# Optimization experiments

Measured on AMD Instinct MI355X. Metric: run time of the kernel, lower is better.

Reference implementation:

```python
import jax, jax.numpy as jnp
import numpy as np

EMBED_DIM = 128
NUM_HEADS = 16
D_K = EMBED_DIM // NUM_HEADS  # n_wires per head = 8
DEPTH = 1
DIM = 2 ** D_K  # 256 state amplitudes


def _cnot_chain_inverse_perm(d, depth):
    """Inverse permutation of basis states under `depth` rounds of the CNOT ladder
    CNOT(0,1),...,CNOT(d-2,d-1),CNOT(d-1,0). Wire 0 = most significant bit."""
    idx = np.arange(2 ** d)
    shifts = d - 1 - np.arange(d)
    bits = (idx[:, None] >> shifts) & 1  # (2^d, d)
    for _ in range(depth):
        for w in range(d - 1):
            bits[:, w + 1] ^= bits[:, w]
        bits[:, 0] ^= bits[:, d - 1]
    fwd = (bits << shifts).sum(axis=1)  # psi'[fwd[b]] = psi[b]
    inv = np.empty_like(fwd)
    inv[fwd] = idx  # psi'[j] = psi[inv[j]]
    return inv


def _pauliz_signs(d):
    idx = np.arange(2 ** d)
    shifts = d - 1 - np.arange(d)
    bits = (idx[:, None] >> shifts) & 1
    return (1.0 - 2.0 * bits).astype(np.float32)  # (2^d, d)


_INV_PERM = jnp.asarray(_cnot_chain_inverse_perm(D_K, DEPTH))
_SIGNS = jnp.asarray(_pauliz_signs(D_K))


def quantum_head(angles):
    """angles: (..., d) RX rotation angles. Returns PauliZ expectations (..., d).

    Product state amplitudes after per-wire RX from |0..0>: probabilities are
    products of cos^2/sin^2; CNOT ladder is a basis permutation; <Z_w> is a
    signed sum of probabilities."""
    half = angles * 0.5
    c2 = jnp.cos(half) ** 2
    s2 = jnp.sin(half) ** 2
    lead = angles.shape[:-1]
    p = jnp.ones(lead + (1,), angles.dtype)
    for w in range(D_K):  # builds (..., 2^d) probability vector
        pair = jnp.stack([c2[..., w], s2[..., w]], axis=-1)
        p = (p[..., :, None] * pair[..., None, :]).reshape(lead + (-1,))
    p = p[..., _INV_PERM]  # apply CNOT ladder permutation
    return p @ _SIGNS  # (..., d) PauliZ expectations


def setup_inputs() -> dict:
    key = jax.random.key(0)
    ks = jax.random.split(key, 10)
    B, S, E = 8, 512, EMBED_DIM
    sc = 1.0 / np.sqrt(E)
    return {
        "x": jax.random.normal(ks[0], (B, S, E), jnp.float32),
        "Wq": jax.random.normal(ks[1], (E, E), jnp.float32) * sc,
        "bq": jnp.zeros((E,), jnp.float32),
        "Wk": jax.random.normal(ks[2], (E, E), jnp.float32) * sc,
        "bk": jnp.zeros((E,), jnp.float32),
        "Wv": jax.random.normal(ks[3], (E, E), jnp.float32) * sc,
        "bv": jnp.zeros((E,), jnp.float32),
        "Wo": jax.random.normal(ks[4], (E, E), jnp.float32) * sc,
        "bo": jnp.zeros((E,), jnp.float32),
        "theta": jax.random.normal(ks[5], (NUM_HEADS, D_K), jnp.float32),
    }


def reference(x, Wq, bq, Wk, bk, Wv, bv, Wo, bo, theta):
    B, S, E = x.shape
    H, dk = NUM_HEADS, D_K

    def split_heads(y):  # (B,S,E) -> (B,H,S,dk)
        return y.reshape(B, S, H, dk).transpose(0, 2, 1, 3)

    q = split_heads(x @ Wq + bq)
    k = split_heads(x @ Wk + bk)
    v = split_heads(x @ Wv + bv)

    th = theta[None, :, None, :]  # broadcast per-head trainable RX angles
    qh = quantum_head(q + th)
    kh = quantum_head(k + th)
    vh = quantum_head(v + th)

    scores = jnp.einsum("bhsd,bhtd->bhst", qh, kh) / jnp.sqrt(jnp.asarray(dk, x.dtype))
    attn = jax.nn.softmax(scores, axis=-1)
    out = jnp.einsum("bhst,bhtd->bhsd", attn, vh)
    out = out.transpose(0, 2, 1, 3).reshape(B, S, E)
    return out @ Wo + bo
```

## Files before the change

### kernel.cpp

```cpp
#include <hip/hip_runtime.h>
#include <hip/hip_bf16.h>
#include <math.h>

#define BB 8
#define SS 512
#define EE 128
#define HH 16
#define DKK 8

#define FMA4(ACC, S, W) do { (ACC).x += (S)*(W).x; (ACC).y += (S)*(W).y; \
                             (ACC).z += (S)*(W).z; (ACC).w += (S)*(W).w; } while(0)

__global__ __launch_bounds__(256) void k_qkvq(
    const float* __restrict__ x,
    const float* __restrict__ Wq, const float* __restrict__ bq,
    const float* __restrict__ Wk, const float* __restrict__ bk,
    const float* __restrict__ Wv, const float* __restrict__ bv,
    const float* __restrict__ theta,
    float* __restrict__ qh, float* __restrict__ kh, float* __restrict__ vh)
{
    __shared__ float xs[16][128];
    const int t = threadIdx.x;
    const int m = blockIdx.y;
    const int row0 = blockIdx.x * 16;

    {
        const float4* xv = (const float4*)(x + (size_t)row0 * 128);
        float4* xsv = (float4*)&xs[0][0];
        xsv[t]       = xv[t];
        xsv[t + 256] = xv[t + 256];
    }
    __syncthreads();

    const int cg   = t & 31;
    const int col0 = cg * 4;
    const int rg   = t >> 5;
    const int r0   = rg * 2;

    const float* __restrict__ W  = (m == 0) ? Wq : (m == 1) ? Wk : Wv;
    const float* __restrict__ bb = (m == 0) ? bq : (m == 1) ? bk : bv;
    float* __restrict__ outp     = (m == 0) ? qh : (m == 1) ? kh : vh;

    float4 acc0 = *(const float4*)&bb[col0];
    float4 acc1 = acc0;

    #pragma unroll 4
    for (int k4 = 0; k4 < 32; ++k4) {
        const float4 xa = ((const float4*)xs[r0 + 0])[k4];
        const float4 xb = ((const float4*)xs[r0 + 1])[k4];
        const float4 w0 = *(const float4*)&W[(k4 * 4 + 0) * 128 + col0];
        const float4 w1 = *(const float4*)&W[(k4 * 4 + 1) * 128 + col0];
        const float4 w2 = *(const float4*)&W[(k4 * 4 + 2) * 128 + col0];
        const float4 w3 = *(const float4*)&W[(k4 * 4 + 3) * 128 + col0];
        FMA4(acc0, xa.x, w0); FMA4(acc0, xa.y, w1);
        FMA4(acc0, xa.z, w2); FMA4(acc0, xa.w, w3);
        FMA4(acc1, xb.x, w0); FMA4(acc1, xb.y, w1);
        FMA4(acc1, xb.z, w2); FMA4(acc1, xb.w, w3);
    }

    const float4 th = *(const float4*)&theta[col0];
    const int h    = cg >> 1;
    const int half = cg & 1;

    float4 accs[2] = {acc0, acc1};
    #pragma unroll
    for (int r = 0; r < 2; ++r) {
        float4 c;
        c.x = __cosf(accs[r].x + th.x);
        c.y = __cosf(accs[r].y + th.y);
        c.z = __cosf(accs[r].z + th.z);
        c.w = __cosf(accs[r].w + th.w);
        const float p0 = c.x;
        const float p1 = p0 * c.y;
        const float p2 = p1 * c.z;
        const float p3 = p2 * c.w;
        const float recv = __shfl_xor(p3, 1);
        float4 o;
        if (half == 0) {
            const float s123 = c.y * c.z * c.w;
            o.x = s123 * recv;
            o.y = p1;
            o.z = p2;
            o.w = p3;
        } else {
            o.x = recv * p0;
            o.y = recv * p1;
            o.z = recv * p2;
            o.w = recv * p3;
        }
        const int g  = row0 + r0 + r;
        const int b_ = g >> 9;
        const int s  = g & 511;
        *(float4*)&outp[(((size_t)b_ * HH + h) * SS + s) * DKK + half * 4] = o;
    }
}

__global__ __launch_bounds__(256) void k_attn(
    const float* __restrict__ qh, const float* __restrict__ kh,
    const float* __restrict__ vh, float* __restrict__ hid)
{
    __shared__ float smem[12288];
    float4* kk = (float4*)smem;
    float4* vv = (float4*)smem + 1024;
    float (*part)[256][12] = (float (*)[256][12])smem;

    const int t  = threadIdx.x;
    const int L  = t & 63;
    const int wv = __builtin_amdgcn_readfirstlane(t >> 6);
    const int bh = blockIdx.x >> 1;
    const int q0 = (blockIdx.x & 1) * 256;
    const int h  = bh & 15;
    const int b_ = bh >> 4;

    {
        const float4* kg = (const float4*)kh + (size_t)bh * 1024;
        const float4* vg = (const float4*)vh + (size_t)bh * 1024;
        #pragma unroll
        for (int i = 0; i < 4; ++i) {
            kk[t + 256 * i] = kg[t + 256 * i];
            vv[t + 256 * i] = vg[t + 256 * i];
        }
    }

    float4 qa[4], qb[4];
    {
        const float4* qg = (const float4*)qh + ((size_t)bh * 512 + q0) * 2;
        #pragma unroll
        for (int rr = 0; rr < 4; ++rr) {
            qa[rr] = qg[(rr * 64 + L) * 2];
            qb[rr] = qg[(rr * 64 + L) * 2 + 1];
        }
    }
    __syncthreads();

    float4 accA[4], accB[4];
    float  den[4];
    #pragma unroll
    for (int rr = 0; rr < 4; ++rr) {
        accA[rr] = make_float4(0.f, 0.f, 0.f, 0.f);
        accB[rr] = make_float4(0.f, 0.f, 0.f, 0.f);
        den[rr]  = 0.f;
    }
    const float scale = 0.35355339059327373f;
    const float4* kbase = kk + wv * 256;
    const float4* vbase = vv + wv * 256;

    #pragma unroll 2
    for (int j = 0; j < 128; ++j) {
        const float4 k0 = kbase[2 * j];
        const float4 k1 = kbase[2 * j + 1];
        const float4 v0 = vbase[2 * j];
        const float4 v1 = vbase[2 * j + 1];
        #pragma unroll
        for (int rr = 0; rr < 4; ++rr) {
            const float s = qa[rr].x*k0.x + qa[rr].y*k0.y + qa[rr].z*k0.z + qa[rr].w*k0.w
                          + qb[rr].x*k1.x + qb[rr].y*k1.y + qb[rr].z*k1.z + qb[rr].w*k1.w;
            const float e = __expf(s * scale);
            den[rr] += e;
            FMA4(accA[rr], e, v0);
            FMA4(accB[rr], e, v1);
        }
    }
    __syncthreads();

    #pragma unroll
    for (int rr = 0; rr < 4; ++rr) {
        float* p = &part[wv][rr * 64 + L][0];
        ((float4*)p)[0] = accA[rr];
        ((float4*)p)[1] = accB[rr];
        p[8] = den[rr];
    }
    __syncthreads();

    {
        float4 rA = make_float4(0.f, 0.f, 0.f, 0.f);
        float4 rB = make_float4(0.f, 0.f, 0.f, 0.f);
        float  rd = 0.f;
        #pragma unroll
        for (int wq = 0; wq < 4; ++wq) {
            const float* p = &part[wq][t][0];
            const float4 a = ((const float4*)p)[0];
            const float4 b = ((const float4*)p)[1];
            rA.x += a.x; rA.y += a.y; rA.z += a.z; rA.w += a.w;
            rB.x += b.x; rB.y += b.y; rB.z += b.z; rB.w += b.w;
            rd   += p[8];
        }
        const float inv = 1.0f / rd;
        rA.x *= inv; rA.y *= inv; rA.z *= inv; rA.w *= inv;
        rB.x *= inv; rB.y *= inv; rB.z *= inv; rB.w *= inv;
        float* o = hid + ((size_t)(b_ * 512 + q0 + t)) * 128 + h * 8;
        ((float4*)o)[0] = rA;
        ((float4*)o)[1] = rB;
    }
}

__global__ __launch_bounds__(256) void k_out(
    const float* __restrict__ hid, const float* __restrict__ Wo,
    const float* __restrict__ bo, float* __restrict__ out)
{
    __shared__ float hs[16][128];
    const int t = threadIdx.x;
    const int row0 = blockIdx.x * 16;

    {
        const float4* hv = (const float4*)(hid + (size_t)row0 * 128);
        float4* hsv = (float4*)&hs[0][0];
        hsv[t]       = hv[t];
        hsv[t + 256] = hv[t + 256];
    }
    __syncthreads();

    const int cg   = t & 31;
    const int col0 = cg * 4;
    const int rg   = t >> 5;
    const int r0   = rg * 2;

    float4 acc0 = *(const float4*)&bo[col0];
    float4 acc1 = acc0;

    #pragma unroll 4
    for (int k4 = 0; k4 < 32; ++k4) {
        const float4 xa = ((const float4*)hs[r0 + 0])[k4];
        const float4 xb = ((const float4*)hs[r0 + 1])[k4];
        const float4 w0 = *(const float4*)&Wo[(k4 * 4 + 0) * 128 + col0];
        const float4 w1 = *(const float4*)&Wo[(k4 * 4 + 1) * 128 + col0];
        const float4 w2 = *(const float4*)&Wo[(k4 * 4 + 2) * 128 + col0];
        const float4 w3 = *(const float4*)&Wo[(k4 * 4 + 3) * 128 + col0];
        FMA4(acc0, xa.x, w0); FMA4(acc0, xa.y, w1);
        FMA4(acc0, xa.z, w2); FMA4(acc0, xa.w, w3);
        FMA4(acc1, xb.x, w0); FMA4(acc1, xb.y, w1);
        FMA4(acc1, xb.z, w2); FMA4(acc1, xb.w, w3);
    }

    *(float4*)&out[(size_t)(row0 + r0 + 0) * 128 + col0] = acc0;
    *(float4*)&out[(size_t)(row0 + r0 + 1) * 128 + col0] = acc1;
}

extern "C" void kernel_launch(void* const* d_in, const int* in_sizes, int n_in,
                              void* d_out, int out_size, void* d_ws, size_t ws_size,
                              hipStream_t stream)
{
    const float* x     = (const float*)d_in[0];
    const float* Wq    = (const float*)d_in[1];
    const float* bq    = (const float*)d_in[2];
    const float* Wk    = (const float*)d_in[3];
    const float* bk    = (const float*)d_in[4];
    const float* Wv    = (const float*)d_in[5];
    const float* bv    = (const float*)d_in[6];
    const float* Wo    = (const float*)d_in[7];
    const float* bo    = (const float*)d_in[8];
    const float* theta = (const float*)d_in[9];
    float* out = (float*)d_out;

    float* ws  = (float*)d_ws;
    float* qh  = ws;
    float* kh  = ws + 524288;
    float* vh  = ws + 1048576;
    float* hid = ws + 1572864;

    k_qkvq<<<dim3(256, 3), 256, 0, stream>>>(x, Wq, bq, Wk, bk, Wv, bv,
                                             theta, qh, kh, vh);
    k_attn<<<256, 256, 0, stream>>>(qh, kh, vh, hid);
    k_out <<<256, 256, 0, stream>>>(hid, Wo, bo, out);
}
```

Baseline: 52.34 us.

## Split attention keys across blocks and merge partial sums in output projection

Attention now launches 512 blocks, each handling a quarter of the keys for all 512 queries of one batch-head. Each wave writes unnormalized partial numerators and denominators to global memory, and the output-projection kernel sums the 16 partials per row before the matmul. The QKV kernel drops its shared-memory staging of x and reads rows directly from global memory, and launch-bounds hints are added. This buys more parallelism for the attention stage, but adds a large partial-sum buffer (about 50 MB written and read back) and raises register pressure from 8 query rows per thread.

```diff
diff --git a/kernel.cpp b/kernel.cpp
--- a/kernel.cpp
+++ b/kernel.cpp
@@ -11,7 +11,7 @@
 #define FMA4(ACC, S, W) do { (ACC).x += (S)*(W).x; (ACC).y += (S)*(W).y; \
                              (ACC).z += (S)*(W).z; (ACC).w += (S)*(W).w; } while(0)
 
-__global__ __launch_bounds__(256) void k_qkvq(
+__global__ __launch_bounds__(256, 3) void k_qkvq(
     const float* __restrict__ x,
     const float* __restrict__ Wq, const float* __restrict__ bq,
     const float* __restrict__ Wk, const float* __restrict__ bk,
@@ -19,18 +19,9 @@
     const float* __restrict__ theta,
     float* __restrict__ qh, float* __restrict__ kh, float* __restrict__ vh)
 {
-    __shared__ float xs[16][128];
     const int t = threadIdx.x;
     const int m = blockIdx.y;
     const int row0 = blockIdx.x * 16;
-
-    {
-        const float4* xv = (const float4*)(x + (size_t)row0 * 128);
-        float4* xsv = (float4*)&xs[0][0];
-        xsv[t]       = xv[t];
-        xsv[t + 256] = xv[t + 256];
-    }
-    __syncthreads();
 
     const int cg   = t & 31;
     const int col0 = cg * 4;
@@ -41,13 +32,15 @@
     const float* __restrict__ bb = (m == 0) ? bq : (m == 1) ? bk : bv;
     float* __restrict__ outp     = (m == 0) ? qh : (m == 1) ? kh : vh;
 
+    const float4* xr = (const float4*)(x + (size_t)(row0 + r0) * 128);
+
     float4 acc0 = *(const float4*)&bb[col0];
     float4 acc1 = acc0;
 
     #pragma unroll 4
     for (int k4 = 0; k4 < 32; ++k4) {
-        const float4 xa = ((const float4*)xs[r0 + 0])[k4];
-        const float4 xb = ((const float4*)xs[r0 + 1])[k4];
+        const float4 xa = xr[k4];
+        const float4 xb = xr[32 + k4];
         const float4 w0 = *(const float4*)&W[(k4 * 4 + 0) * 128 + col0];
         const float4 w1 = *(const float4*)&W[(k4 * 4 + 1) * 128 + col0];
         const float4 w2 = *(const float4*)&W[(k4 * 4 + 2) * 128 + col0];
@@ -95,107 +88,81 @@
     }
 }
 
-__global__ __launch_bounds__(256) void k_attn(
+__global__ __launch_bounds__(256, 2) void k_attn(
     const float* __restrict__ qh, const float* __restrict__ kh,
-    const float* __restrict__ vh, float* __restrict__ hid)
-{
-    __shared__ float smem[12288];
-    float4* kk = (float4*)smem;
-    float4* vv = (float4*)smem + 1024;
-    float (*part)[256][12] = (float (*)[256][12])smem;
+    const float* __restrict__ vh, float* __restrict__ part)
+{
+    __shared__ float4 kk[256];
+    __shared__ float4 vv[256];
 
     const int t  = threadIdx.x;
     const int L  = t & 63;
     const int wv = __builtin_amdgcn_readfirstlane(t >> 6);
-    const int bh = blockIdx.x >> 1;
-    const int q0 = (blockIdx.x & 1) * 256;
-    const int h  = bh & 15;
-    const int b_ = bh >> 4;
-
-    {
-        const float4* kg = (const float4*)kh + (size_t)bh * 1024;
-        const float4* vg = (const float4*)vh + (size_t)bh * 1024;
+    const int bh = blockIdx.x >> 2;
+    const int jq = blockIdx.x & 3;
+
+    {
+        const float4* kg = (const float4*)kh + (size_t)bh * 1024 + jq * 256;
+        const float4* vg = (const float4*)vh + (size_t)bh * 1024 + jq * 256;
+        kk[t] = kg[t];
+        vv[t] = vg[t];
+    }
+
+    float4 qa[8], qb[8];
+    {
+        const float4* qg = (const float4*)qh + (size_t)bh * 1024;
         #pragma unroll
-        for (int i = 0; i < 4; ++i) {
-            kk[t + 256 * i] = kg[t + 256 * i];
-            vv[t + 256 * i] = vg[t + 256 * i];
-        }
-    }
-
-    float4 qa[4], qb[4];
-    {
-        const float4* qg = (const float4*)qh + ((size_t)bh * 512 + q0) * 2;
-        #pragma unroll
-        for (int rr = 0; rr < 4; ++rr) {
-            qa[rr] = qg[(rr * 64 + L) * 2];
-            qb[rr] = qg[(rr * 64 + L) * 2 + 1];
+        for (int r = 0; r < 8; ++r) {
+            qa[r] = qg[(r * 64 + L) * 2];
+            qb[r] = qg[(r * 64 + L) * 2 + 1];
         }
     }
     __syncthreads();
 
-    float4 accA[4], accB[4];
-    float  den[4];
+    float4 accA[8], accB[8];
+    float  den[8];
     #pragma unroll
-    for (int rr = 0; rr < 4; ++rr) {
-        accA[rr] = make_float4(0.f, 0.f, 0.f, 0.f);
-        accB[rr] = make_float4(0.f, 0.f, 0.f, 0.f);
-        den[rr]  = 0.f;
+    for (int r = 0; r < 8; ++r) {
+        accA[r] = make_float4(0.f, 0.f, 0.f, 0.f);
+        accB[r] = make_float4(0.f, 0.f, 0.f, 0.f);
+        den[r]  = 0.f;
     }
     const float scale = 0.35355339059327373f;
-    const float4* kbase = kk + wv * 256;
-    const float4* vbase = vv + wv * 256;
+    const float4* kbase = kk + wv * 64;
+    const float4* vbase = vv + wv * 64;
 
     #pragma unroll 2
-    for (int j = 0; j < 128; ++j) {
+    for (int j = 0; j < 32; ++j) {
         const float4 k0 = kbase[2 * j];
         const float4 k1 = kbase[2 * j + 1];
         const float4 v0 = vbase[2 * j];
         const float4 v1 = vbase[2 * j + 1];
         #pragma unroll
-        for (int rr = 0; rr < 4; ++rr) {
-            const float s = qa[rr].x*k0.x + qa[rr].y*k0.y + qa[rr].z*k0.z + qa[rr].w*k0.w
-                          + qb[rr].x*k1.x + qb[rr].y*k1.y + qb[rr].z*k1.z + qb[rr].w*k1.w;
+        for (int r = 0; r < 8; ++r) {
+            const float s = qa[r].x*k0.x + qa[r].y*k0.y + qa[r].z*k0.z + qa[r].w*k0.w
+                          + qb[r].x*k1.x + qb[r].y*k1.y + qb[r].z*k1.z + qb[r].w*k1.w;
             const float e = __expf(s * scale);
-            den[rr] += e;
-            FMA4(accA[rr], e, v0);
-            FMA4(accB[rr], e, v1);
-        }
-    }
-    __syncthreads();
-
-    #pragma unroll
-    for (int rr = 0; rr < 4; ++rr) {
-        float* p = &part[wv][rr * 64 + L][0];
-        ((float4*)p)[0] = accA[rr];
-        ((float4*)p)[1] = accB[rr];
-        p[8] = den[rr];
-    }
-    __syncthreads();
-
-    {
-        float4 rA = make_float4(0.f, 0.f, 0.f, 0.f);
-        float4 rB = make_float4(0.f, 0.f, 0.f, 0.f);
-        float  rd = 0.f;
+            den[r] += e;
+            FMA4(accA[r], e, v0);
+            FMA4(accB[r], e, v1);
+        }
+    }
+
+    {
+        float4* pf4 = (float4*)part;
+        const size_t slotbase = ((size_t)bh * 16 + jq * 4 + wv) * 512;
         #pragma unroll
-        for (int wq = 0; wq < 4; ++wq) {
-            const float* p = &part[wq][t][0];
-            const float4 a = ((const float4*)p)[0];
-            const float4 b = ((const float4*)p)[1];
-            rA.x += a.x; rA.y += a.y; rA.z += a.z; rA.w += a.w;
-            rB.x += b.x; rB.y += b.y; rB.z += b.z; rB.w += b.w;
-            rd   += p[8];
-        }
-        const float inv = 1.0f / rd;
-        rA.x *= inv; rA.y *= inv; rA.z *= inv; rA.w *= inv;
-        rB.x *= inv; rB.y *= inv; rB.z *= inv; rB.w *= inv;
-        float* o = hid + ((size_t)(b_ * 512 + q0 + t)) * 128 + h * 8;
-        ((float4*)o)[0] = rA;
-        ((float4*)o)[1] = rB;
+        for (int r = 0; r < 8; ++r) {
+            const size_t o = (slotbase + r * 64 + L) * 3;
+            pf4[o]     = accA[r];
+            pf4[o + 1] = accB[r];
+            pf4[o + 2] = make_float4(den[r], 0.f, 0.f, 0.f);
+        }
     }
 }
 
 __global__ __launch_bounds__(256) void k_out(
-    const float* __restrict__ hid, const float* __restrict__ Wo,
+    const float* __restrict__ part, const float* __restrict__ Wo,
     const float* __restrict__ bo, float* __restrict__ out)
 {
     __shared__ float hs[16][128];
@@ -203,10 +170,31 @@
     const int row0 = blockIdx.x * 16;
 
     {
-        const float4* hv = (const float4*)(hid + (size_t)row0 * 128);
-        float4* hsv = (float4*)&hs[0][0];
-        hsv[t]       = hv[t];
-        hsv[t + 256] = hv[t + 256];
+        const int rt = t >> 4;
+        const int h  = t & 15;
+        const int g  = row0 + rt;
+        const int b_ = g >> 9;
+        const int s  = g & 511;
+        const float4* pf4 = (const float4*)part;
+        const size_t base = (((size_t)(b_ * 16 + h)) * 16) * 512 + s;
+        float4 nA = make_float4(0.f, 0.f, 0.f, 0.f);
+        float4 nB = make_float4(0.f, 0.f, 0.f, 0.f);
+        float  dn = 0.f;
+        #pragma unroll 4
+        for (int p = 0; p < 16; ++p) {
+            const size_t o = (base + (size_t)p * 512) * 3;
+            const float4 a = pf4[o];
+            const float4 b = pf4[o + 1];
+            const float4 d = pf4[o + 2];
+            nA.x += a.x; nA.y += a.y; nA.z += a.z; nA.w += a.w;
+            nB.x += b.x; nB.y += b.y; nB.z += b.z; nB.w += b.w;
+            dn   += d.x;
+        }
+        const float inv = 1.0f / dn;
+        nA.x *= inv; nA.y *= inv; nA.z *= inv; nA.w *= inv;
+        nB.x *= inv; nB.y *= inv; nB.z *= inv; nB.w *= inv;
+        *(float4*)&hs[rt][h * 8]     = nA;
+        *(float4*)&hs[rt][h * 8 + 4] = nB;
     }
     __syncthreads();
 
@@ -252,14 +240,14 @@
     const float* theta = (const float*)d_in[9];
     float* out = (float*)d_out;
 
-    float* ws  = (float*)d_ws;
-    float* qh  = ws;
-    float* kh  = ws + 524288;
-    float* vh  = ws + 1048576;
-    float* hid = ws + 1572864;
+    float* ws   = (float*)d_ws;
+    float* qh   = ws;
+    float* kh   = ws + 524288;
+    float* vh   = ws + 1048576;
+    float* part = ws + 1572864;
 
     k_qkvq<<<dim3(256, 3), 256, 0, stream>>>(x, Wq, bq, Wk, bk, Wv, bv,
                                              theta, qh, kh, vh);
-    k_attn<<<256, 256, 0, stream>>>(qh, kh, vh, hid);
-    k_out <<<256, 256, 0, stream>>>(hid, Wo, bo, out);
-}
+    k_attn<<<512, 256, 0, stream>>>(qh, kh, vh, part);
+    k_out <<<256, 256, 0, stream>>>(part, Wo, bo, out);
+}
```

After: 68.20 us. 1.3x slower.

## Increase grid parallelism in attention and output kernels, drop shared-memory staging

Applied to the files above, without the earlier changes.

The attention kernel now launches 1024 blocks, one per (batch, head, 64-query tile). Each thread owns a single query and streams K/V straight from global memory instead of staging them in LDS, and the hid layout becomes head-major. The output projection gathers that head-major hid into 8-row tiles across 512 blocks, and the QKV kernel reads x directly from global memory instead of through shared memory. The aim is more blocks across the many CUs and less LDS/sync overhead, at the cost of K/V being re-read from L2 by four times as many blocks and less register reuse per thread.

```diff
diff --git a/kernel.cpp b/kernel.cpp
--- a/kernel.cpp
+++ b/kernel.cpp
@@ -19,18 +19,9 @@
     const float* __restrict__ theta,
     float* __restrict__ qh, float* __restrict__ kh, float* __restrict__ vh)
 {
-    __shared__ float xs[16][128];
     const int t = threadIdx.x;
     const int m = blockIdx.y;
     const int row0 = blockIdx.x * 16;
-
-    {
-        const float4* xv = (const float4*)(x + (size_t)row0 * 128);
-        float4* xsv = (float4*)&xs[0][0];
-        xsv[t]       = xv[t];
-        xsv[t + 256] = xv[t + 256];
-    }
-    __syncthreads();
 
     const int cg   = t & 31;
     const int col0 = cg * 4;
@@ -41,13 +32,15 @@
     const float* __restrict__ bb = (m == 0) ? bq : (m == 1) ? bk : bv;
     float* __restrict__ outp     = (m == 0) ? qh : (m == 1) ? kh : vh;
 
+    const float4* xr = (const float4*)(x + (size_t)(row0 + r0) * 128);
+
     float4 acc0 = *(const float4*)&bb[col0];
     float4 acc1 = acc0;
 
     #pragma unroll 4
     for (int k4 = 0; k4 < 32; ++k4) {
-        const float4 xa = ((const float4*)xs[r0 + 0])[k4];
-        const float4 xb = ((const float4*)xs[r0 + 1])[k4];
+        const float4 xa = xr[k4];
+        const float4 xb = xr[32 + k4];
         const float4 w0 = *(const float4*)&W[(k4 * 4 + 0) * 128 + col0];
         const float4 w1 = *(const float4*)&W[(k4 * 4 + 1) * 128 + col0];
         const float4 w2 = *(const float4*)&W[(k4 * 4 + 2) * 128 + col0];
@@ -99,98 +92,65 @@
     const float* __restrict__ qh, const float* __restrict__ kh,
     const float* __restrict__ vh, float* __restrict__ hid)
 {
-    __shared__ float smem[12288];
-    float4* kk = (float4*)smem;
-    float4* vv = (float4*)smem + 1024;
-    float (*part)[256][12] = (float (*)[256][12])smem;
+    __shared__ float part[4][64][12];
 
     const int t  = threadIdx.x;
     const int L  = t & 63;
-    const int wv = __builtin_amdgcn_readfirstlane(t >> 6);
-    const int bh = blockIdx.x >> 1;
-    const int q0 = (blockIdx.x & 1) * 256;
-    const int h  = bh & 15;
-    const int b_ = bh >> 4;
-
-    {
-        const float4* kg = (const float4*)kh + (size_t)bh * 1024;
-        const float4* vg = (const float4*)vh + (size_t)bh * 1024;
-        #pragma unroll
-        for (int i = 0; i < 4; ++i) {
-            kk[t + 256 * i] = kg[t + 256 * i];
-            vv[t + 256 * i] = vg[t + 256 * i];
-        }
-    }
-
-    float4 qa[4], qb[4];
-    {
-        const float4* qg = (const float4*)qh + ((size_t)bh * 512 + q0) * 2;
-        #pragma unroll
-        for (int rr = 0; rr < 4; ++rr) {
-            qa[rr] = qg[(rr * 64 + L) * 2];
-            qb[rr] = qg[(rr * 64 + L) * 2 + 1];
-        }
-    }
-    __syncthreads();
-
-    float4 accA[4], accB[4];
-    float  den[4];
-    #pragma unroll
-    for (int rr = 0; rr < 4; ++rr) {
-        accA[rr] = make_float4(0.f, 0.f, 0.f, 0.f);
-        accB[rr] = make_float4(0.f, 0.f, 0.f, 0.f);
-        den[rr]  = 0.f;
-    }
+    const int wv = t >> 6;
+    const int bh = blockIdx.x & 127;
+    const int q0 = (blockIdx.x >> 7) * 64;
+
+    const float4* qg = (const float4*)qh + ((size_t)bh * 512 + q0 + L) * 2;
+    const float4 qa = qg[0];
+    const float4 qb = qg[1];
+
+    const float4* kbase = (const float4*)kh + ((size_t)bh * 512 + wv * 128) * 2;
+    const float4* vbase = (const float4*)vh + ((size_t)bh * 512 + wv * 128) * 2;
+
+    float4 accA = make_float4(0.f, 0.f, 0.f, 0.f);
+    float4 accB = make_float4(0.f, 0.f, 0.f, 0.f);
+    float  den  = 0.f;
     const float scale = 0.35355339059327373f;
-    const float4* kbase = kk + wv * 256;
-    const float4* vbase = vv + wv * 256;
-
-    #pragma unroll 2
+
+    #pragma unroll 4
     for (int j = 0; j < 128; ++j) {
         const float4 k0 = kbase[2 * j];
         const float4 k1 = kbase[2 * j + 1];
         const float4 v0 = vbase[2 * j];
         const float4 v1 = vbase[2 * j + 1];
-        #pragma unroll
-        for (int rr = 0; rr < 4; ++rr) {
-            const float s = qa[rr].x*k0.x + qa[rr].y*k0.y + qa[rr].z*k0.z + qa[rr].w*k0.w
-                          + qb[rr].x*k1.x + qb[rr].y*k1.y + qb[rr].z*k1.z + qb[rr].w*k1.w;
-            const float e = __expf(s * scale);
-            den[rr] += e;
-            FMA4(accA[rr], e, v0);
-            FMA4(accB[rr], e, v1);
-        }
-    }
+        const float s = qa.x*k0.x + qa.y*k0.y + qa.z*k0.z + qa.w*k0.w
+                      + qb.x*k1.x + qb.y*k1.y + qb.z*k1.z + qb.w*k1.w;
+        const float e = __expf(s * scale);
+        den += e;
+        FMA4(accA, e, v0);
+        FMA4(accB, e, v1);
+    }
+
+    float* p = &part[wv][L][0];
+    ((float4*)p)[0] = accA;
+    ((float4*)p)[1] = accB;
+    p[8] = den;
     __syncthreads();
 
-    #pragma unroll
-    for (int rr = 0; rr < 4; ++rr) {
-        float* p = &part[wv][rr * 64 + L][0];
-        ((float4*)p)[0] = accA[rr];
-        ((float4*)p)[1] = accB[rr];
-        p[8] = den[rr];
-    }
-    __syncthreads();
-
-    {
+    if (t < 64) {
         float4 rA = make_float4(0.f, 0.f, 0.f, 0.f);
         float4 rB = make_float4(0.f, 0.f, 0.f, 0.f);
         float  rd = 0.f;
         #pragma unroll
         for (int wq = 0; wq < 4; ++wq) {
-            const float* p = &part[wq][t][0];
-            const float4 a = ((const float4*)p)[0];
-            const float4 b = ((const float4*)p)[1];
+            const float* pp = &part[wq][t][0];
+            const float4 a = ((const float4*)pp)[0];
+            const float4 b = ((const float4*)pp)[1];
             rA.x += a.x; rA.y += a.y; rA.z += a.z; rA.w += a.w;
             rB.x += b.x; rB.y += b.y; rB.z += b.z; rB.w += b.w;
-            rd   += p[8];
+            rd   += pp[8];
         }
         const float inv = 1.0f / rd;
         rA.x *= inv; rA.y *= inv; rA.z *= inv; rA.w *= inv;
         rB.x *= inv; rB.y *= inv; rB.z *= inv; rB.w *= inv;
-        float* o = hid + ((size_t)(b_ * 512 + q0 + t)) * 128 + h * 8;
-        ((float4*)o)[0] = rA;
-        ((float4*)o)[1] = rB;
+        float4* o = (float4*)hid + ((size_t)bh * 512 + q0 + t) * 2;
+        o[0] = rA;
+        o[1] = rB;
     }
 }
 
@@ -198,42 +158,41 @@
     const float* __restrict__ hid, const float* __restrict__ Wo,
     const float* __restrict__ bo, float* __restrict__ out)
 {
-    __shared__ float hs[16][128];
+    __shared__ float hs[8][128];
     const int t = threadIdx.x;
-    const int row0 = blockIdx.x * 16;
+    const int row0 = blockIdx.x * 8;
 
     {
-        const float4* hv = (const float4*)(hid + (size_t)row0 * 128);
-        float4* hsv = (float4*)&hs[0][0];
-        hsv[t]       = hv[t];
-        hsv[t + 256] = hv[t + 256];
+        const int u    = t >> 1;
+        const int half = t & 1;
+        const int row  = u >> 4;
+        const int h    = u & 15;
+        const int g    = row0 + row;
+        const int b_   = g >> 9;
+        const int s    = g & 511;
+        const float4 v = ((const float4*)hid)[(((size_t)b_ * HH + h) * SS + s) * 2 + half];
+        *(float4*)&hs[row][h * 8 + half * 4] = v;
     }
     __syncthreads();
 
     const int cg   = t & 31;
     const int col0 = cg * 4;
-    const int rg   = t >> 5;
-    const int r0   = rg * 2;
-
-    float4 acc0 = *(const float4*)&bo[col0];
-    float4 acc1 = acc0;
+    const int rr   = t >> 5;
+
+    float4 acc = *(const float4*)&bo[col0];
 
     #pragma unroll 4
     for (int k4 = 0; k4 < 32; ++k4) {
-        const float4 xa = ((const float4*)hs[r0 + 0])[k4];
-        const float4 xb = ((const float4*)hs[r0 + 1])[k4];
+        const float4 xa = ((const float4*)hs[rr])[k4];
         const float4 w0 = *(const float4*)&Wo[(k4 * 4 + 0) * 128 + col0];
         const float4 w1 = *(const float4*)&Wo[(k4 * 4 + 1) * 128 + col0];
         const float4 w2 = *(const float4*)&Wo[(k4 * 4 + 2) * 128 + col0];
         const float4 w3 = *(const float4*)&Wo[(k4 * 4 + 3) * 128 + col0];
-        FMA4(acc0, xa.x, w0); FMA4(acc0, xa.y, w1);
-        FMA4(acc0, xa.z, w2); FMA4(acc0, xa.w, w3);
-        FMA4(acc1, xb.x, w0); FMA4(acc1, xb.y, w1);
-        FMA4(acc1, xb.z, w2); FMA4(acc1, xb.w, w3);
-    }
-
-    *(float4*)&out[(size_t)(row0 + r0 + 0) * 128 + col0] = acc0;
-    *(float4*)&out[(size_t)(row0 + r0 + 1) * 128 + col0] = acc1;
+        FMA4(acc, xa.x, w0); FMA4(acc, xa.y, w1);
+        FMA4(acc, xa.z, w2); FMA4(acc, xa.w, w3);
+    }
+
+    *(float4*)&out[(size_t)(row0 + rr) * 128 + col0] = acc;
 }
 
 extern "C" void kernel_launch(void* const* d_in, const int* in_sizes, int n_in,
@@ -260,6 +219,6 @@
 
     k_qkvq<<<dim3(256, 3), 256, 0, stream>>>(x, Wq, bq, Wk, bk, Wv, bv,
                                              theta, qh, kh, vh);
-    k_attn<<<256, 256, 0, stream>>>(qh, kh, vh, hid);
-    k_out <<<256, 256, 0, stream>>>(hid, Wo, bo, out);
-}
+    k_attn<<<1024, 256, 0, stream>>>(qh, kh, vh, hid);
+    k_out <<<512, 256, 0, stream>>>(hid, Wo, bo, out);
+}
```

After: 92.72 us. 1.77x slower.

## Split attention key loop across eight waves per block with two-stage reduction

Applied to the files above, without the earlier changes.

The attention kernel now launches 512-thread blocks, so each of eight waves processes a 64-key slice instead of a 128-key slice, doubling parallelism per block. Partial softmax numerators and denominators are combined in shared memory in two stages before the final normalisation. The softmax scale is folded into the q vectors up front, and launch_bounds occupancy hints are added to the other kernels. The cost is extra synchronisation and shared-memory reduction traffic, plus higher register pressure constraints from the bounds.

```diff
diff --git a/kernel.cpp b/kernel.cpp
--- a/kernel.cpp
+++ b/kernel.cpp
@@ -10,8 +10,9 @@
 
 #define FMA4(ACC, S, W) do { (ACC).x += (S)*(W).x; (ACC).y += (S)*(W).y; \
                              (ACC).z += (S)*(W).z; (ACC).w += (S)*(W).w; } while(0)
-
-__global__ __launch_bounds__(256) void k_qkvq(
+#define DOT4(A, B) ((A).x*(B).x + (A).y*(B).y + (A).z*(B).z + (A).w*(B).w)
+
+__global__ __launch_bounds__(256, 4) void k_qkvq(
     const float* __restrict__ x,
     const float* __restrict__ Wq, const float* __restrict__ bq,
     const float* __restrict__ Wk, const float* __restrict__ bk,
@@ -95,106 +96,125 @@
     }
 }
 
-__global__ __launch_bounds__(256) void k_attn(
+__global__ __launch_bounds__(512, 4) void k_attn(
     const float* __restrict__ qh, const float* __restrict__ kh,
     const float* __restrict__ vh, float* __restrict__ hid)
 {
-    __shared__ float smem[12288];
-    float4* kk = (float4*)smem;
-    float4* vv = (float4*)smem + 1024;
-    float (*part)[256][12] = (float (*)[256][12])smem;
+    __shared__ float4 smem[3072];
+    float4* kk = smem;
+    float4* vv = smem + 1024;
 
     const int t  = threadIdx.x;
     const int L  = t & 63;
-    const int wv = __builtin_amdgcn_readfirstlane(t >> 6);
-    const int bh = blockIdx.x >> 1;
-    const int q0 = (blockIdx.x & 1) * 256;
-    const int h  = bh & 15;
-    const int b_ = bh >> 4;
+    const int wv = t >> 6;
+    const int bh = blockIdx.x & 127;
+    const int q0 = (blockIdx.x >> 7) * 256;
 
     {
         const float4* kg = (const float4*)kh + (size_t)bh * 1024;
         const float4* vg = (const float4*)vh + (size_t)bh * 1024;
-        #pragma unroll
-        for (int i = 0; i < 4; ++i) {
-            kk[t + 256 * i] = kg[t + 256 * i];
-            vv[t + 256 * i] = vg[t + 256 * i];
-        }
-    }
-
+        kk[t]       = kg[t];
+        kk[t + 512] = kg[t + 512];
+        vv[t]       = vg[t];
+        vv[t + 512] = vg[t + 512];
+    }
+
+    const float scale = 0.35355339059327373f;
     float4 qa[4], qb[4];
     {
         const float4* qg = (const float4*)qh + ((size_t)bh * 512 + q0) * 2;
         #pragma unroll
-        for (int rr = 0; rr < 4; ++rr) {
-            qa[rr] = qg[(rr * 64 + L) * 2];
-            qb[rr] = qg[(rr * 64 + L) * 2 + 1];
-        }
-    }
-    __syncthreads();
-
-    float4 accA[4], accB[4];
+        for (int r = 0; r < 4; ++r) {
+            float4 a = qg[(L + 64 * r) * 2];
+            float4 b = qg[(L + 64 * r) * 2 + 1];
+            a.x *= scale; a.y *= scale; a.z *= scale; a.w *= scale;
+            b.x *= scale; b.y *= scale; b.z *= scale; b.w *= scale;
+            qa[r] = a; qb[r] = b;
+        }
+    }
+    __syncthreads();
+
+    float4 aA[4], aB[4];
     float  den[4];
     #pragma unroll
-    for (int rr = 0; rr < 4; ++rr) {
-        accA[rr] = make_float4(0.f, 0.f, 0.f, 0.f);
-        accB[rr] = make_float4(0.f, 0.f, 0.f, 0.f);
-        den[rr]  = 0.f;
-    }
-    const float scale = 0.35355339059327373f;
-    const float4* kbase = kk + wv * 256;
-    const float4* vbase = vv + wv * 256;
-
-    #pragma unroll 2
-    for (int j = 0; j < 128; ++j) {
+    for (int r = 0; r < 4; ++r) {
+        aA[r] = make_float4(0.f, 0.f, 0.f, 0.f);
+        aB[r] = make_float4(0.f, 0.f, 0.f, 0.f);
+        den[r] = 0.f;
+    }
+
+    const float4* kbase = kk + wv * 128;
+    const float4* vbase = vv + wv * 128;
+
+    #pragma unroll 4
+    for (int j = 0; j < 64; ++j) {
         const float4 k0 = kbase[2 * j];
         const float4 k1 = kbase[2 * j + 1];
         const float4 v0 = vbase[2 * j];
         const float4 v1 = vbase[2 * j + 1];
         #pragma unroll
-        for (int rr = 0; rr < 4; ++rr) {
-            const float s = qa[rr].x*k0.x + qa[rr].y*k0.y + qa[rr].z*k0.z + qa[rr].w*k0.w
-                          + qb[rr].x*k1.x + qb[rr].y*k1.y + qb[rr].z*k1.z + qb[rr].w*k1.w;
-            const float e = __expf(s * scale);
-            den[rr] += e;
-            FMA4(accA[rr], e, v0);
-            FMA4(accB[rr], e, v1);
-        }
-    }
-    __syncthreads();
-
-    #pragma unroll
-    for (int rr = 0; rr < 4; ++rr) {
-        float* p = &part[wv][rr * 64 + L][0];
-        ((float4*)p)[0] = accA[rr];
-        ((float4*)p)[1] = accB[rr];
-        p[8] = den[rr];
-    }
-    __syncthreads();
-
-    {
-        float4 rA = make_float4(0.f, 0.f, 0.f, 0.f);
-        float4 rB = make_float4(0.f, 0.f, 0.f, 0.f);
-        float  rd = 0.f;
-        #pragma unroll
-        for (int wq = 0; wq < 4; ++wq) {
-            const float* p = &part[wq][t][0];
-            const float4 a = ((const float4*)p)[0];
-            const float4 b = ((const float4*)p)[1];
+        for (int r = 0; r < 4; ++r) {
+            const float s = DOT4(qa[r], k0) + DOT4(qb[r], k1);
+            const float e = __expf(s);
+            den[r] += e;
+            FMA4(aA[r], e, v0);
+            FMA4(aB[r], e, v1);
+        }
+    }
+
+    __syncthreads();
+
+    float4* part = smem;
+    if (wv < 4) {
+        #pragma unroll
+        for (int r = 0; r < 4; ++r) {
+            const int idx = (wv * 256 + L + 64 * r) * 3;
+            part[idx]     = aA[r];
+            part[idx + 1] = aB[r];
+            part[idx + 2] = make_float4(den[r], 0.f, 0.f, 0.f);
+        }
+    }
+    __syncthreads();
+    if (wv >= 4) {
+        #pragma unroll
+        for (int r = 0; r < 4; ++r) {
+            const int idx = ((wv - 4) * 256 + L + 64 * r) * 3;
+            float4 pa = part[idx];
+            float4 pb = part[idx + 1];
+            float4 pd = part[idx + 2];
+            pa.x += aA[r].x; pa.y += aA[r].y; pa.z += aA[r].z; pa.w += aA[r].w;
+            pb.x += aB[r].x; pb.y += aB[r].y; pb.z += aB[r].z; pb.w += aB[r].w;
+            pd.x += den[r];
+            part[idx]     = pa;
+            part[idx + 1] = pb;
+            part[idx + 2] = pd;
+        }
+    }
+    __syncthreads();
+
+    if (t < 256) {
+        float4 rA = make_float4(0.f, 0.f, 0.f, 0.f), rB = rA;
+        float rd = 0.f;
+        #pragma unroll
+        for (int w = 0; w < 4; ++w) {
+            const int idx = (w * 256 + t) * 3;
+            const float4 a = part[idx];
+            const float4 b = part[idx + 1];
             rA.x += a.x; rA.y += a.y; rA.z += a.z; rA.w += a.w;
             rB.x += b.x; rB.y += b.y; rB.z += b.z; rB.w += b.w;
-            rd   += p[8];
+            rd   += part[idx + 2].x;
         }
         const float inv = 1.0f / rd;
         rA.x *= inv; rA.y *= inv; rA.z *= inv; rA.w *= inv;
         rB.x *= inv; rB.y *= inv; rB.z *= inv; rB.w *= inv;
-        float* o = hid + ((size_t)(b_ * 512 + q0 + t)) * 128 + h * 8;
+        const int b_ = bh >> 4, h = bh & 15;
+        float* o = hid + ((size_t)(b_ * 512) + q0 + t) * 128 + h * 8;
         ((float4*)o)[0] = rA;
         ((float4*)o)[1] = rB;
     }
 }
 
-__global__ __launch_bounds__(256) void k_out(
+__global__ __launch_bounds__(256, 4) void k_out(
     const float* __restrict__ hid, const float* __restrict__ Wo,
     const float* __restrict__ bo, float* __restrict__ out)
 {
@@ -260,6 +280,6 @@
 
     k_qkvq<<<dim3(256, 3), 256, 0, stream>>>(x, Wq, bq, Wk, bk, Wv, bv,
                                              theta, qh, kh, vh);
-    k_attn<<<256, 256, 0, stream>>>(qh, kh, vh, hid);
+    k_attn<<<256, 512, 0, stream>>>(qh, kh, vh, hid);
     k_out <<<256, 256, 0, stream>>>(hid, Wo, bo, out);
 }
```

Measured after the change: 46.01 us. -12.1%, faster.
